# Optimization experiments

Measured on AMD Instinct MI355X. Metric: run time of the kernel, lower is better.

## Reference

```python
import jax, jax.numpy as jnp
import numpy as np

B, NPG, DEG = 128, 400, 16
N, E = B * NPG, B * NPG * DEG
E_PER = E // B
K1, K2, K3 = 360, 324, 292  # ceil(0.9*400), ceil(0.9*360), ceil(0.9*324)
EPS = 1e-5


def setup_inputs() -> dict:
    key = jax.random.key(0)
    ks = jax.random.split(key, 48)
    # edges constrained within each graph (contiguous equal-size graphs)
    g = jnp.repeat(jnp.arange(B, dtype=jnp.int32), E_PER)
    src = jax.random.randint(ks[0], (E,), 0, NPG, dtype=jnp.int32) + g * NPG
    dst = jax.random.randint(ks[1], (E,), 0, NPG, dtype=jnp.int32) + g * NPG
    inp = {
        'x': jax.random.normal(ks[2], (N, 64), dtype=jnp.float32),
        'edge_index': jnp.stack([src, dst]),
        'batch': jnp.repeat(jnp.arange(B, dtype=jnp.int32), NPG),
    }
    def glorot(k, a, b):
        lim = float(np.sqrt(6.0 / (a + b)))
        return jax.random.uniform(k, (a, b), minval=-lim, maxval=lim, dtype=jnp.float32)
    conv_dims = [(64, 32), (32, 64), (64, 128), (128, 128)]
    for i, (a, b) in enumerate(conv_dims, 1):
        inp[f'W{i}'] = glorot(ks[2 + i], a, b)
        inp[f'b{i}'] = jnp.zeros((b,), jnp.float32)
    for i, d in zip((1, 2, 3), (32, 64, 128)):
        inp[f'p{i}'] = jax.random.uniform(ks[8 + i], (d,), minval=-1.0, maxval=1.0, dtype=jnp.float32) / float(np.sqrt(d))
    lin_dims = [(128, 64), (64, 64), (64, 32), (32, 16), (16, 1)]
    for i, (a, b) in enumerate(lin_dims, 1):
        inp[f'Lw{i}'] = glorot(ks[12 + i], a, b)
        inp[f'Lb{i}'] = jnp.zeros((b,), jnp.float32)
    for i, d in enumerate((64, 64, 32, 16), 1):
        inp[f'g{i}'] = jnp.ones((d,), jnp.float32)
        inp[f'be{i}'] = jnp.zeros((d,), jnp.float32)
    return inp


def _gcn(x, src, dst, emask, nmask, W, b):
    h = x @ W
    deg = nmask + jax.ops.segment_sum(emask, dst, num_segments=N)
    dinv = jnp.where(deg > 0, jax.lax.rsqrt(deg), 0.0)
    norm = dinv[src] * dinv[dst] * emask
    agg = jax.ops.segment_sum(h[src] * norm[:, None], dst, num_segments=N)
    agg = agg + h * (dinv * dinv * nmask)[:, None]  # self-loop term
    return (agg + b) * nmask[:, None]


def _topk_pool(x, nmask, p, k):
    # PyG TopKPooling: score = x.p/||p||, keep top-k per graph, x *= tanh(score)
    score = (x @ p) / jnp.linalg.norm(p)
    sel = jnp.where(nmask > 0, score, -jnp.inf).reshape(B, NPG)
    _, idx = jax.lax.top_k(sel, k)
    gidx = (idx + (jnp.arange(B) * NPG)[:, None]).reshape(-1)
    new_mask = jnp.zeros((N,), x.dtype).at[gidx].set(1.0)
    return x * (jnp.tanh(score) * new_mask)[:, None], new_mask


def reference(x, edge_index, batch, W1, b1, p1, W2, b2, p2, W3, b3, p3, W4, b4,
              Lw1, Lb1, Lw2, Lb2, Lw3, Lb3, Lw4, Lb4, Lw5, Lb5,
              g1, be1, g2, be2, g3, be3, g4, be4):
    src, dst = edge_index[0], edge_index[1]
    nmask = jnp.ones((N,), jnp.float32)
    emask = jnp.ones((E,), jnp.float32)
    x = jax.nn.relu(_gcn(x, src, dst, emask, nmask, W1, b1))
    x, nmask = _topk_pool(x, nmask, p1, K1)
    emask = emask * nmask[src] * nmask[dst]
    x = jax.nn.relu(_gcn(x, src, dst, emask, nmask, W2, b2))
    x, nmask = _topk_pool(x, nmask, p2, K2)
    emask = emask * nmask[src] * nmask[dst]
    x = jax.nn.relu(_gcn(x, src, dst, emask, nmask, W3, b3))
    x, nmask = _topk_pool(x, nmask, p3, K3)
    emask = emask * nmask[src] * nmask[dst]
    x = jax.nn.relu(_gcn(x, src, dst, emask, nmask, W4, b4))
    h = x.reshape(B, NPG, -1).max(axis=1)
    def lin_bn(h, W, bb, ga, be):
        h = h @ W + bb
        m = h.mean(0)
        v = h.var(0)  # biased, matches BatchNorm1d training normalization
        return jax.nn.relu(ga * (h - m) / jnp.sqrt(v + EPS) + be)
    h = lin_bn(h, Lw1, Lb1, g1, be1)
    h = lin_bn(h, Lw2, Lb2, g2, be2)
    h = lin_bn(h, Lw3, Lb3, g3, be3)
    h = lin_bn(h, Lw4, Lb4, g4, be4)
    return h @ Lw5 + Lb5
```

## Files before the change

kernel.cpp:

```cpp
#include <hip/hip_runtime.h>
#include <math.h>

#define NNODES 51200
#define BGRAPHS 128
#define NPG 400
#define NEDGES 819200
#define EPG 6400
#define SLP 7680

__global__ __launch_bounds__(512) void csr_build_kernel(
    const int* __restrict__ src, const int* __restrict__ dst,
    unsigned short* __restrict__ slg, int* __restrict__ gsg, int* __restrict__ gcg,
    float* __restrict__ nmask, float* __restrict__ dinv, float* __restrict__ sc,
    float* __restrict__ hp) {
    __shared__ int deg[NPG];
    __shared__ int incl[512];
    __shared__ int gs[NPG];
    __shared__ int cur[NPG];
    const int g = blockIdx.x, t = threadIdx.x;
    for (int i = t; i < NPG; i += 512) deg[i] = 0;
    if (t < 128) hp[g * 128 + t] = 0.0f;
    __syncthreads();
    for (int e = t; e < EPG; e += 512)
        atomicAdd(&deg[dst[g * EPG + e] - g * NPG], 1);
    __syncthreads();
    const int d = (t < NPG) ? deg[t] : 0;
    const int p = (d + 3) >> 2;
    incl[t] = p;
    __syncthreads();
    for (int off = 1; off < 512; off <<= 1) {
        int add = (t >= off) ? incl[t - off] : 0;
        __syncthreads();
        incl[t] += add;
        __syncthreads();
    }
    if (t < NPG) {
        const int gstart = incl[t] - p;
        gs[t] = gstart;
        gsg[g * NPG + t] = gstart;
        gcg[g * NPG + t] = p;
        cur[t] = gstart * 4;
        nmask[g * NPG + t] = 1.0f;
        const float dv = rsqrtf(1.0f + (float)d);
        dinv[g * NPG + t] = dv;
        sc[g * NPG + t] = dv;
    }
    __syncthreads();
    for (int e = t; e < EPG; e += 512) {
        int dl = dst[g * EPG + e] - g * NPG;
        int pos = atomicAdd(&cur[dl], 1);
        slg[g * SLP + pos] = (unsigned short)(src[g * EPG + e] - g * NPG);
    }
    __syncthreads();
    if (t < NPG) {
        const int end = (gs[t] + p) * 4;
        for (int i = cur[t]; i < end; i++) slg[g * SLP + i] = (unsigned short)NPG;
    }
}

template<int IN, int OUT, int MODE>
__global__ __launch_bounds__(256) void gemm_kernel(
    const float* __restrict__ X, const float* __restrict__ W,
    const float* __restrict__ bias, const float* __restrict__ nmask,
    float* __restrict__ H, const float* __restrict__ p,
    float* __restrict__ score, float* __restrict__ hp) {
    __shared__ __align__(16) float sX[64 * IN];
    __shared__ unsigned smax[256];
    const int row0 = blockIdx.x * 64;
    const int t = threadIdx.x;
    for (int i = t; i < 64 * IN / 4; i += 256)
        reinterpret_cast<float4*>(sX)[i] =
            reinterpret_cast<const float4*>(X + (size_t)row0 * IN)[i];
    if (MODE == 3) smax[t] = 0u;
    __syncthreads();
    constexpr int CG  = OUT / 4;
    constexpr int RG  = 256 / CG;
    constexpr int RPT = 64 / RG;
    const int c0 = (t % CG) * 4;
    const int r0 = (t / CG) * RPT;
    float acc[RPT][4];
#pragma unroll
    for (int r = 0; r < RPT; r++)
#pragma unroll
        for (int j = 0; j < 4; j++) acc[r][j] = 0.0f;
    for (int k4 = 0; k4 < IN / 4; k4++) {
        const float4 w0 = *reinterpret_cast<const float4*>(&W[(k4 * 4 + 0) * OUT + c0]);
        const float4 w1 = *reinterpret_cast<const float4*>(&W[(k4 * 4 + 1) * OUT + c0]);
        const float4 w2 = *reinterpret_cast<const float4*>(&W[(k4 * 4 + 2) * OUT + c0]);
        const float4 w3 = *reinterpret_cast<const float4*>(&W[(k4 * 4 + 3) * OUT + c0]);
#pragma unroll
        for (int r = 0; r < RPT; r++) {
            const float4 xv = *reinterpret_cast<const float4*>(&sX[(r0 + r) * IN + k4 * 4]);
            acc[r][0] += xv.x * w0.x + xv.y * w1.x + xv.z * w2.x + xv.w * w3.x;
            acc[r][1] += xv.x * w0.y + xv.y * w1.y + xv.z * w2.y + xv.w * w3.y;
            acc[r][2] += xv.x * w0.z + xv.y * w1.z + xv.z * w2.z + xv.w * w3.z;
            acc[r][3] += xv.x * w0.w + xv.y * w1.w + xv.z * w2.w + xv.w * w3.w;
        }
    }
    const int graph0 = row0 / 400;
    const int bnd = (graph0 + 1) * 400;
    float ps[RPT];
    float cmax[4] = {0.f, 0.f, 0.f, 0.f};
#pragma unroll
    for (int r = 0; r < RPT; r++) {
        const int row = row0 + r0 + r;
        float4 v = make_float4(acc[r][0], acc[r][1], acc[r][2], acc[r][3]);
        if (MODE >= 2) {
            const float4 b4 = *reinterpret_cast<const float4*>(&bias[c0]);
            const float m = nmask[row];
            v.x = fmaxf(v.x + b4.x, 0.0f) * m;
            v.y = fmaxf(v.y + b4.y, 0.0f) * m;
            v.z = fmaxf(v.z + b4.z, 0.0f) * m;
            v.w = fmaxf(v.w + b4.w, 0.0f) * m;
        }
        if (MODE != 3) *reinterpret_cast<float4*>(&H[(size_t)row * OUT + c0]) = v;
        if (MODE == 2) {
            const float4 p4 = *reinterpret_cast<const float4*>(&p[c0]);
            ps[r] = v.x * p4.x + v.y * p4.y + v.z * p4.z + v.w * p4.w;
        }
        if (MODE == 3) {
            cmax[0] = fmaxf(cmax[0], v.x);
            cmax[1] = fmaxf(cmax[1], v.y);
            cmax[2] = fmaxf(cmax[2], v.z);
            cmax[3] = fmaxf(cmax[3], v.w);
        }
    }
    if (MODE == 2) {
#pragma unroll
        for (int r = 0; r < RPT; r++) {
#pragma unroll
            for (int off = 1; off < CG; off <<= 1) ps[r] += __shfl_xor(ps[r], off);
        }
        if ((t % CG) == 0) {
#pragma unroll
            for (int r = 0; r < RPT; r++) score[row0 + r0 + r] = ps[r];
        }
    }
    if (MODE == 3) {
        const int seg = ((row0 + r0) >= bnd) ? 1 : 0;
        atomicMax(&smax[seg * 128 + c0 + 0], __float_as_uint(cmax[0]));
        atomicMax(&smax[seg * 128 + c0 + 1], __float_as_uint(cmax[1]));
        atomicMax(&smax[seg * 128 + c0 + 2], __float_as_uint(cmax[2]));
        atomicMax(&smax[seg * 128 + c0 + 3], __float_as_uint(cmax[3]));
        __syncthreads();
        unsigned* hpu = reinterpret_cast<unsigned*>(hp);
        if (t < 128) atomicMax(&hpu[graph0 * 128 + t], smax[t]);
        const int graph1 = (row0 + 63) / 400;
        if (graph1 != graph0 && t < 128) atomicMax(&hpu[graph1 * 128 + t], smax[128 + t]);
    }
}

template<int OUT, int NCH, int NS, bool EPI, bool SCORE, bool TOPK>
__global__ __launch_bounds__(512) void gcn_agg_kernel(
    const float* __restrict__ H, float* __restrict__ Y,
    const float* __restrict__ dinv_g, const float* __restrict__ sc_g,
    const float* __restrict__ bias,
    const float* __restrict__ p_sc, float* __restrict__ score_out,
    const float* __restrict__ scoreb_in, const float* __restrict__ nmask_in,
    float* __restrict__ nmask_out, const float* __restrict__ p_pool,
    int K, int PDIM,
    const unsigned short* __restrict__ slg, const int* __restrict__ gsg,
    const int* __restrict__ gcg) {
    __shared__ __align__(16) float Hl[(NPG + 1) * 36];
    __shared__ float dinvl[NPG];
    __shared__ float scl[NPG];
    __shared__ int gsl[NPG];
    __shared__ int gcl[NPG];
    __shared__ unsigned long long sl64[SLP / 4];
    __shared__ float misc[4];
    const unsigned short* sl = reinterpret_cast<const unsigned short*>(sl64);
    const int b   = blockIdx.x;
    const int g   = b / (NCH * NS);
    const int rem = b % (NCH * NS);
    const int f0  = (rem / NS) * 32;
    const int n0  = (rem % NS) * (NPG / NS);
    const int t   = threadIdx.x;

    for (int i = t; i < NPG; i += 512) {
        gsl[i] = gsg[g * NPG + i];
        gcl[i] = gcg[g * NPG + i];
    }
    for (int i = t; i < SLP / 4; i += 512)
        sl64[i] = reinterpret_cast<const unsigned long long*>(slg + (size_t)g * SLP)[i];

    if (TOPK) {
        float* sval = Hl;
        int*   sidx = (int*)(Hl + 512);
        float* sraw = Hl + 1024;
        float* nml  = Hl + 1440;
        if (t < 64) {
            float s = 0.0f;
            for (int j = t; j < PDIM; j += 64) s += p_pool[j] * p_pool[j];
#pragma unroll
            for (int o = 32; o > 0; o >>= 1) s += __shfl_xor(s, o, 64);
            if (t == 0) misc[0] = sqrtf(s);
        }
        float v = -INFINITY;
        int ix = t;
        if (t < NPG) {
            const float raw = scoreb_in[g * NPG + t];
            sraw[t] = raw;
            v = (nmask_in[g * NPG + t] > 0.0f) ? raw : -INFINITY;
        }
        __syncthreads();
        for (int kk = 2; kk <= 512; kk <<= 1) {
            for (int j = kk >> 1; j > 0; j >>= 1) {
                float vb; int ib;
                if (j >= 64) {
                    sval[t] = v; sidx[t] = ix;
                    __syncthreads();
                    vb = sval[t ^ j]; ib = sidx[t ^ j];
                    __syncthreads();
                } else {
                    vb = __shfl_xor(v, j, 64);
                    ib = __shfl_xor(ix, j, 64);
                }
                const bool ownFirst = (v > vb) || (v == vb && ix < ib);
                const bool lower = (t & j) == 0;
                const bool desc = (t & kk) == 0;
                const bool keepOwn = lower ? (desc == ownFirst) : (desc != ownFirst);
                if (!keepOwn) { v = vb; ix = ib; }
            }
        }
        if (t <= NPG) nml[t] = 0.0f;
        __syncthreads();
        if (t < K) nml[ix] = 1.0f;
        __syncthreads();
        if (rem == 0 && t < NPG) nmask_out[g * NPG + t] = nml[t];
        const float spn = misc[0];
        for (int n = t; n < NPG; n += 512) {
            float dv = 0.0f;
            if (nml[n] > 0.0f) {
                float d = 1.0f;
                const int g0 = gsl[n], g1 = g0 + gcl[n];
                for (int gg = g0; gg < g1; ++gg) {
                    const unsigned long long q = *reinterpret_cast<const unsigned long long*>(&sl[gg * 4]);
                    d += nml[(int)(q & 0xFFFF)] + nml[(int)((q >> 16) & 0xFFFF)] +
                         nml[(int)((q >> 32) & 0xFFFF)] + nml[(int)(q >> 48)];
                }
                dv = rsqrtf(d);
            }
            dinvl[n] = dv;
            scl[n] = (nml[n] > 0.0f) ? tanhf(sraw[n] / spn) * dv : 0.0f;
        }
        __syncthreads();
    } else {
        for (int i = t; i < NPG; i += 512) {
            dinvl[i] = dinv_g[g * NPG + i];
            scl[i]   = sc_g[g * NPG + i];
        }
        __syncthreads();
    }

    for (int i = t; i < NPG * 8; i += 512) {
        const int n = i >> 3, q = i & 7;
        const float s = scl[n];
        float4 v = *reinterpret_cast<const float4*>(&H[(size_t)(g * NPG + n) * OUT + f0 + q * 4]);
        v.x *= s; v.y *= s; v.z *= s; v.w *= s;
        *reinterpret_cast<float4*>(&Hl[n * 36 + q * 4]) = v;
    }
    if (t < 36) Hl[NPG * 36 + t] = 0.0f;
    __syncthreads();

    const int wave = t >> 6, lane = t & 63;
    const int sub = lane >> 3, f4 = lane & 7;
    constexpr int NPB = NPG / NS;
    for (int n = n0 + wave * 8 + sub; n < n0 + NPB; n += 64) {
        const float di = dinvl[n];
        if (di == 0.0f) continue;
        const int g0 = gsl[n], g1 = g0 + gcl[n];
        float4 acc = *reinterpret_cast<const float4*>(&Hl[n * 36 + f4 * 4]);
        for (int gg = g0; gg < g1; ++gg) {
            const unsigned long long q = *reinterpret_cast<const unsigned long long*>(&sl[gg * 4]);
            const int s0 = (int)(q & 0xFFFF), s1 = (int)((q >> 16) & 0xFFFF);
            const int s2 = (int)((q >> 32) & 0xFFFF), s3 = (int)(q >> 48);
            const float4 a = *reinterpret_cast<const float4*>(&Hl[s0 * 36 + f4 * 4]);
            const float4 bb = *reinterpret_cast<const float4*>(&Hl[s1 * 36 + f4 * 4]);
            const float4 c = *reinterpret_cast<const float4*>(&Hl[s2 * 36 + f4 * 4]);
            const float4 dd = *reinterpret_cast<const float4*>(&Hl[s3 * 36 + f4 * 4]);
            acc.x += (a.x + bb.x) + (c.x + dd.x);
            acc.y += (a.y + bb.y) + (c.y + dd.y);
            acc.z += (a.z + bb.z) + (c.z + dd.z);
            acc.w += (a.w + bb.w) + (c.w + dd.w);
        }
        acc.x *= di; acc.y *= di; acc.z *= di; acc.w *= di;
        if (EPI) {
            const float4 b4 = *reinterpret_cast<const float4*>(&bias[f0 + f4 * 4]);
            acc.x = fmaxf(acc.x + b4.x, 0.0f);
            acc.y = fmaxf(acc.y + b4.y, 0.0f);
            acc.z = fmaxf(acc.z + b4.z, 0.0f);
            acc.w = fmaxf(acc.w + b4.w, 0.0f);
        }
        *reinterpret_cast<float4*>(&Y[(size_t)(g * NPG + n) * OUT + f0 + f4 * 4]) = acc;
        if (SCORE) {
            const float4 p4 = *reinterpret_cast<const float4*>(&p_sc[f4 * 4]);
            float part = acc.x * p4.x + acc.y * p4.y + acc.z * p4.z + acc.w * p4.w;
            part += __shfl_xor(part, 1);
            part += __shfl_xor(part, 2);
            part += __shfl_xor(part, 4);
            if (f4 == 0) score_out[g * NPG + n] = part;
        }
    }
}

template<int IN, int OUT>
__global__ __launch_bounds__(128) void head_layer_kernel(
    const float* __restrict__ A, const float* __restrict__ W,
    const float* __restrict__ b, const float* __restrict__ ga,
    const float* __restrict__ be, float* __restrict__ Y) {
    __shared__ float Al[128 * (IN + 1)];
    __shared__ float red[4];
    const int c = blockIdx.x, t = threadIdx.x;
    for (int i = t; i < 128 * IN; i += 128)
        Al[(i / IN) * (IN + 1) + (i % IN)] = A[i];
    __syncthreads();
    float acc = b[c];
#pragma unroll
    for (int j = 0; j < IN; j++) acc += Al[t * (IN + 1) + j] * W[j * OUT + c];
    float s1 = acc, s2 = acc * acc;
    for (int o = 32; o > 0; o >>= 1) {
        s1 += __shfl_down(s1, o, 64);
        s2 += __shfl_down(s2, o, 64);
    }
    if ((t & 63) == 0) { red[t >> 6] = s1; red[2 + (t >> 6)] = s2; }
    __syncthreads();
    const float S1 = red[0] + red[1], S2 = red[2] + red[3];
    const float m = S1 * (1.0f / 128.0f);
    const float var = S2 * (1.0f / 128.0f) - m * m;
    float val = ga[c] * (acc - m) * rsqrtf(var + 1e-5f) + be[c];
    Y[t * OUT + c] = fmaxf(val, 0.0f);
}

__global__ __launch_bounds__(128) void head_final_kernel(
    const float* __restrict__ A, const float* __restrict__ w,
    const float* __restrict__ b, float* __restrict__ out) {
    const int t = threadIdx.x;
    float acc = b[0];
#pragma unroll
    for (int j = 0; j < 16; j++) acc += A[t * 16 + j] * w[j];
    out[t] = acc;
}

extern "C" void kernel_launch(void* const* d_in, const int* in_sizes, int n_in,
                              void* d_out, int out_size, void* d_ws, size_t ws_size,
                              hipStream_t stream) {
    (void)in_sizes; (void)n_in; (void)out_size; (void)ws_size;
    const float* x   = (const float*)d_in[0];
    const int*   ei  = (const int*)d_in[1];
    const float* W1  = (const float*)d_in[3];  const float* b1  = (const float*)d_in[4];
    const float* W2  = (const float*)d_in[5];  const float* b2  = (const float*)d_in[6];
    const float* W3  = (const float*)d_in[7];  const float* b3  = (const float*)d_in[8];
    const float* W4  = (const float*)d_in[9];  const float* b4  = (const float*)d_in[10];
    const float* p1  = (const float*)d_in[11];
    const float* p2  = (const float*)d_in[12];
    const float* p3  = (const float*)d_in[13];
    const float* Lw1 = (const float*)d_in[14]; const float* Lb1 = (const float*)d_in[15];
    const float* Lw2 = (const float*)d_in[16]; const float* Lb2 = (const float*)d_in[17];
    const float* Lw3 = (const float*)d_in[18]; const float* Lb3 = (const float*)d_in[19];
    const float* Lw4 = (const float*)d_in[20]; const float* Lb4 = (const float*)d_in[21];
    const float* Lw5 = (const float*)d_in[22]; const float* Lb5 = (const float*)d_in[23];
    const float* g1  = (const float*)d_in[24]; const float* be1 = (const float*)d_in[25];
    const float* g2  = (const float*)d_in[26]; const float* be2 = (const float*)d_in[27];
    const float* g3  = (const float*)d_in[28]; const float* be3 = (const float*)d_in[29];
    const float* g4  = (const float*)d_in[30]; const float* be4 = (const float*)d_in[31];

    const int* src = ei;
    const int* dst = ei + NEDGES;

    float* ws    = (float*)d_ws;
    float* hb    = ws;
    float* x0    = hb + (size_t)NNODES * 128;
    float* x1    = x0 + (size_t)NNODES * 128;
    float* nmA   = x1 + (size_t)NNODES * 128;
    float* nmB   = nmA + NNODES;
    float* dinv  = nmB + NNODES;
    float* sc    = dinv + NNODES;
    float* scoreb= sc + NNODES;
    float* hp    = scoreb + NNODES;
    float* a1    = hp + 128 * 128;
    float* a2    = a1 + 128 * 64;
    float* a3    = a2 + 128 * 64;
    float* a4    = a3 + 128 * 32;
    unsigned short* slg = (unsigned short*)(a4 + 128 * 16);
    int* gsg = (int*)(slg + (size_t)BGRAPHS * SLP);
    int* gcg = gsg + (size_t)BGRAPHS * NPG;

    csr_build_kernel<<<BGRAPHS, 512, 0, stream>>>(src, dst, slg, gsg, gcg, nmA, dinv, sc, hp);

    gemm_kernel<64, 32, 0><<<NNODES / 64, 256, 0, stream>>>(x, W1, nullptr, nullptr, hb, nullptr, nullptr, nullptr);
    gcn_agg_kernel<32, 1, 2, true, true, false><<<BGRAPHS * 2, 512, 0, stream>>>(
        hb, x0, dinv, sc, b1, p1, scoreb,
        nullptr, nullptr, nullptr, nullptr, 0, 0, slg, gsg, gcg);

    gcn_agg_kernel<32, 1, 2, false, false, true><<<BGRAPHS * 2, 512, 0, stream>>>(
        x0, hb, nullptr, nullptr, nullptr, nullptr, nullptr,
        scoreb, nmA, nmB, p1, 360, 32, slg, gsg, gcg);
    gemm_kernel<32, 64, 2><<<NNODES / 64, 256, 0, stream>>>(hb, W2, b2, nmB, x1, p2, scoreb, nullptr);

    gcn_agg_kernel<64, 2, 2, false, false, true><<<BGRAPHS * 4, 512, 0, stream>>>(
        x1, hb, nullptr, nullptr, nullptr, nullptr, nullptr,
        scoreb, nmB, nmA, p2, 324, 64, slg, gsg, gcg);
    gemm_kernel<64, 128, 2><<<NNODES / 64, 256, 0, stream>>>(hb, W3, b3, nmA, x0, p3, scoreb, nullptr);

    gcn_agg_kernel<128, 4, 1, false, false, true><<<BGRAPHS * 4, 512, 0, stream>>>(
        x0, hb, nullptr, nullptr, nullptr, nullptr, nullptr,
        scoreb, nmA, nmB, p3, 292, 128, slg, gsg, gcg);
    gemm_kernel<128, 128, 3><<<NNODES / 64, 256, 0, stream>>>(hb, W4, b4, nmB, x1, nullptr, nullptr, hp);

    head_layer_kernel<128, 64><<<64, 128, 0, stream>>>(hp, Lw1, Lb1, g1, be1, a1);
    head_layer_kernel<64, 64><<<64, 128, 0, stream>>>(a1, Lw2, Lb2, g2, be2, a2);
    head_layer_kernel<64, 32><<<32, 128, 0, stream>>>(a2, Lw3, Lb3, g3, be3, a3);
    head_layer_kernel<32, 16><<<16, 128, 0, stream>>>(a3, Lw4, Lb4, g4, be4, a4);
    head_final_kernel<<<1, 128, 0, stream>>>(a4, Lw5, Lb5, (float*)d_out);
}
```

Measured before the change: 197.1 us.

## Fuse conv2 pooling/aggregation with W2 GEMM and merge head tail layers

Adds a conv2 fused kernel that does the top-k pool, degree normalisation, neighbour aggregation and the 32x64 GEMM with bias, ReLU and score in one block per half-graph. The aggregated result stays in shared memory, so the intermediate write/read of hb and one launch are removed. The order changes from GEMM-then-aggregate to aggregate-then-GEMM, which is linear and therefore equivalent. Score buffers are double-buffered to avoid aliasing. The last three head layers (two linear+BN and the final linear) are merged into one single-block kernel to cut launch overhead. The cost is that the top-k sort and degree computation are now repeated in both half-graph blocks.

```diff
diff --git a/kernel.cpp b/kernel.cpp
--- a/kernel.cpp
+++ b/kernel.cpp
@@ -7,6 +7,9 @@
 #define NEDGES 819200
 #define EPG 6400
 #define SLP 7680
+
+__device__ __forceinline__ float4 ld4(const float* p) { return *reinterpret_cast<const float4*>(p); }
+__device__ __forceinline__ void st4(float* p, float4 v) { *reinterpret_cast<float4*>(p) = v; }
 
 __global__ __launch_bounds__(512) void csr_build_kernel(
     const int* __restrict__ src, const int* __restrict__ dst,
@@ -84,13 +87,13 @@
 #pragma unroll
         for (int j = 0; j < 4; j++) acc[r][j] = 0.0f;
     for (int k4 = 0; k4 < IN / 4; k4++) {
-        const float4 w0 = *reinterpret_cast<const float4*>(&W[(k4 * 4 + 0) * OUT + c0]);
-        const float4 w1 = *reinterpret_cast<const float4*>(&W[(k4 * 4 + 1) * OUT + c0]);
-        const float4 w2 = *reinterpret_cast<const float4*>(&W[(k4 * 4 + 2) * OUT + c0]);
-        const float4 w3 = *reinterpret_cast<const float4*>(&W[(k4 * 4 + 3) * OUT + c0]);
+        const float4 w0 = ld4(&W[(k4 * 4 + 0) * OUT + c0]);
+        const float4 w1 = ld4(&W[(k4 * 4 + 1) * OUT + c0]);
+        const float4 w2 = ld4(&W[(k4 * 4 + 2) * OUT + c0]);
+        const float4 w3 = ld4(&W[(k4 * 4 + 3) * OUT + c0]);
 #pragma unroll
         for (int r = 0; r < RPT; r++) {
-            const float4 xv = *reinterpret_cast<const float4*>(&sX[(r0 + r) * IN + k4 * 4]);
+            const float4 xv = ld4(&sX[(r0 + r) * IN + k4 * 4]);
             acc[r][0] += xv.x * w0.x + xv.y * w1.x + xv.z * w2.x + xv.w * w3.x;
             acc[r][1] += xv.x * w0.y + xv.y * w1.y + xv.z * w2.y + xv.w * w3.y;
             acc[r][2] += xv.x * w0.z + xv.y * w1.z + xv.z * w2.z + xv.w * w3.z;
@@ -106,16 +109,16 @@
         const int row = row0 + r0 + r;
         float4 v = make_float4(acc[r][0], acc[r][1], acc[r][2], acc[r][3]);
         if (MODE >= 2) {
-            const float4 b4 = *reinterpret_cast<const float4*>(&bias[c0]);
+            const float4 b4 = ld4(&bias[c0]);
             const float m = nmask[row];
             v.x = fmaxf(v.x + b4.x, 0.0f) * m;
             v.y = fmaxf(v.y + b4.y, 0.0f) * m;
             v.z = fmaxf(v.z + b4.z, 0.0f) * m;
             v.w = fmaxf(v.w + b4.w, 0.0f) * m;
         }
-        if (MODE != 3) *reinterpret_cast<float4*>(&H[(size_t)row * OUT + c0]) = v;
+        if (MODE != 3) st4(&H[(size_t)row * OUT + c0], v);
         if (MODE == 2) {
-            const float4 p4 = *reinterpret_cast<const float4*>(&p[c0]);
+            const float4 p4 = ld4(&p[c0]);
             ps[r] = v.x * p4.x + v.y * p4.y + v.z * p4.z + v.w * p4.w;
         }
         if (MODE == 3) {
@@ -255,9 +258,9 @@
     for (int i = t; i < NPG * 8; i += 512) {
         const int n = i >> 3, q = i & 7;
         const float s = scl[n];
-        float4 v = *reinterpret_cast<const float4*>(&H[(size_t)(g * NPG + n) * OUT + f0 + q * 4]);
+        float4 v = ld4(&H[(size_t)(g * NPG + n) * OUT + f0 + q * 4]);
         v.x *= s; v.y *= s; v.z *= s; v.w *= s;
-        *reinterpret_cast<float4*>(&Hl[n * 36 + q * 4]) = v;
+        st4(&Hl[n * 36 + q * 4], v);
     }
     if (t < 36) Hl[NPG * 36 + t] = 0.0f;
     __syncthreads();
@@ -269,15 +272,15 @@
         const float di = dinvl[n];
         if (di == 0.0f) continue;
         const int g0 = gsl[n], g1 = g0 + gcl[n];
-        float4 acc = *reinterpret_cast<const float4*>(&Hl[n * 36 + f4 * 4]);
+        float4 acc = ld4(&Hl[n * 36 + f4 * 4]);
         for (int gg = g0; gg < g1; ++gg) {
             const unsigned long long q = *reinterpret_cast<const unsigned long long*>(&sl[gg * 4]);
             const int s0 = (int)(q & 0xFFFF), s1 = (int)((q >> 16) & 0xFFFF);
             const int s2 = (int)((q >> 32) & 0xFFFF), s3 = (int)(q >> 48);
-            const float4 a = *reinterpret_cast<const float4*>(&Hl[s0 * 36 + f4 * 4]);
-            const float4 bb = *reinterpret_cast<const float4*>(&Hl[s1 * 36 + f4 * 4]);
-            const float4 c = *reinterpret_cast<const float4*>(&Hl[s2 * 36 + f4 * 4]);
-            const float4 dd = *reinterpret_cast<const float4*>(&Hl[s3 * 36 + f4 * 4]);
+            const float4 a = ld4(&Hl[s0 * 36 + f4 * 4]);
+            const float4 bb = ld4(&Hl[s1 * 36 + f4 * 4]);
+            const float4 c = ld4(&Hl[s2 * 36 + f4 * 4]);
+            const float4 dd = ld4(&Hl[s3 * 36 + f4 * 4]);
             acc.x += (a.x + bb.x) + (c.x + dd.x);
             acc.y += (a.y + bb.y) + (c.y + dd.y);
             acc.z += (a.z + bb.z) + (c.z + dd.z);
@@ -285,20 +288,181 @@
         }
         acc.x *= di; acc.y *= di; acc.z *= di; acc.w *= di;
         if (EPI) {
-            const float4 b4 = *reinterpret_cast<const float4*>(&bias[f0 + f4 * 4]);
+            const float4 b4 = ld4(&bias[f0 + f4 * 4]);
             acc.x = fmaxf(acc.x + b4.x, 0.0f);
             acc.y = fmaxf(acc.y + b4.y, 0.0f);
             acc.z = fmaxf(acc.z + b4.z, 0.0f);
             acc.w = fmaxf(acc.w + b4.w, 0.0f);
         }
-        *reinterpret_cast<float4*>(&Y[(size_t)(g * NPG + n) * OUT + f0 + f4 * 4]) = acc;
+        st4(&Y[(size_t)(g * NPG + n) * OUT + f0 + f4 * 4], acc);
         if (SCORE) {
-            const float4 p4 = *reinterpret_cast<const float4*>(&p_sc[f4 * 4]);
+            const float4 p4 = ld4(&p_sc[f4 * 4]);
             float part = acc.x * p4.x + acc.y * p4.y + acc.z * p4.z + acc.w * p4.w;
             part += __shfl_xor(part, 1);
             part += __shfl_xor(part, 2);
             part += __shfl_xor(part, 4);
             if (f4 == 0) score_out[g * NPG + n] = part;
+        }
+    }
+}
+
+__global__ __launch_bounds__(512) void conv2_fused_kernel(
+    const float* __restrict__ X0, float* __restrict__ X1,
+    const float* __restrict__ scoreb_in, const float* __restrict__ nmask_in,
+    float* __restrict__ nmask_out, float* __restrict__ scoreb_out,
+    const float* __restrict__ p_pool,
+    const float* __restrict__ W2, const float* __restrict__ b2,
+    const float* __restrict__ p2,
+    const unsigned short* __restrict__ slg, const int* __restrict__ gsg,
+    const int* __restrict__ gcg) {
+    __shared__ __align__(16) float Hl[(NPG + 1) * 36];
+    __shared__ __align__(16) float out2[200 * 36];
+    __shared__ float dinvl[NPG];
+    __shared__ float scl[NPG];
+    __shared__ int gsl[NPG];
+    __shared__ int gcl[NPG];
+    __shared__ unsigned long long sl64[SLP / 4];
+    __shared__ float misc[4];
+    const unsigned short* sl = reinterpret_cast<const unsigned short*>(sl64);
+    const int b = blockIdx.x, g = b >> 1, seg = b & 1;
+    const int n0 = seg * 200;
+    const int t = threadIdx.x;
+
+    for (int i = t; i < NPG; i += 512) {
+        gsl[i] = gsg[g * NPG + i];
+        gcl[i] = gcg[g * NPG + i];
+    }
+    for (int i = t; i < SLP / 4; i += 512)
+        sl64[i] = reinterpret_cast<const unsigned long long*>(slg + (size_t)g * SLP)[i];
+
+    {
+        float* sval = Hl;
+        int*   sidx = (int*)(Hl + 512);
+        float* sraw = Hl + 1024;
+        float* nml  = Hl + 1440;
+        if (t < 64) {
+            float s = 0.0f;
+            for (int j = t; j < 32; j += 64) s += p_pool[j] * p_pool[j];
+#pragma unroll
+            for (int o = 32; o > 0; o >>= 1) s += __shfl_xor(s, o, 64);
+            if (t == 0) misc[0] = sqrtf(s);
+        }
+        float v = -INFINITY;
+        int ix = t;
+        if (t < NPG) {
+            const float raw = scoreb_in[g * NPG + t];
+            sraw[t] = raw;
+            v = (nmask_in[g * NPG + t] > 0.0f) ? raw : -INFINITY;
+        }
+        __syncthreads();
+        for (int kk = 2; kk <= 512; kk <<= 1) {
+            for (int j = kk >> 1; j > 0; j >>= 1) {
+                float vb; int ib;
+                if (j >= 64) {
+                    sval[t] = v; sidx[t] = ix;
+                    __syncthreads();
+                    vb = sval[t ^ j]; ib = sidx[t ^ j];
+                    __syncthreads();
+                } else {
+                    vb = __shfl_xor(v, j, 64);
+                    ib = __shfl_xor(ix, j, 64);
+                }
+                const bool ownFirst = (v > vb) || (v == vb && ix < ib);
+                const bool lower = (t & j) == 0;
+                const bool desc = (t & kk) == 0;
+                const bool keepOwn = lower ? (desc == ownFirst) : (desc != ownFirst);
+                if (!keepOwn) { v = vb; ix = ib; }
+            }
+        }
+        if (t <= NPG) nml[t] = 0.0f;
+        __syncthreads();
+        if (t < 360) nml[ix] = 1.0f;
+        __syncthreads();
+        if (seg == 0 && t < NPG) nmask_out[g * NPG + t] = nml[t];
+        const float spn = misc[0];
+        for (int n = t; n < NPG; n += 512) {
+            float dv = 0.0f;
+            if (nml[n] > 0.0f) {
+                float d = 1.0f;
+                const int g0 = gsl[n], g1 = g0 + gcl[n];
+                for (int gg = g0; gg < g1; ++gg) {
+                    const unsigned long long q = *reinterpret_cast<const unsigned long long*>(&sl[gg * 4]);
+                    d += nml[(int)(q & 0xFFFF)] + nml[(int)((q >> 16) & 0xFFFF)] +
+                         nml[(int)((q >> 32) & 0xFFFF)] + nml[(int)(q >> 48)];
+                }
+                dv = rsqrtf(d);
+            }
+            dinvl[n] = dv;
+            scl[n] = (nml[n] > 0.0f) ? tanhf(sraw[n] / spn) * dv : 0.0f;
+        }
+        __syncthreads();
+    }
+
+    for (int i = t; i < NPG * 8; i += 512) {
+        const int n = i >> 3, q = i & 7;
+        const float s = scl[n];
+        float4 v = ld4(&X0[(size_t)(g * NPG + n) * 32 + q * 4]);
+        v.x *= s; v.y *= s; v.z *= s; v.w *= s;
+        st4(&Hl[n * 36 + q * 4], v);
+    }
+    if (t < 36) Hl[NPG * 36 + t] = 0.0f;
+    __syncthreads();
+
+    {
+        const int wave = t >> 6, lane = t & 63;
+        const int sub = lane >> 3, f4 = lane & 7;
+        for (int n = n0 + wave * 8 + sub; n < n0 + 200; n += 64) {
+            const float di = dinvl[n];
+            float4 acc = make_float4(0.f, 0.f, 0.f, 0.f);
+            if (di != 0.0f) {
+                acc = ld4(&Hl[n * 36 + f4 * 4]);
+                const int g0 = gsl[n], g1 = g0 + gcl[n];
+                for (int gg = g0; gg < g1; ++gg) {
+                    const unsigned long long q = *reinterpret_cast<const unsigned long long*>(&sl[gg * 4]);
+                    const int s0 = (int)(q & 0xFFFF), s1 = (int)((q >> 16) & 0xFFFF);
+                    const int s2 = (int)((q >> 32) & 0xFFFF), s3 = (int)(q >> 48);
+                    const float4 a = ld4(&Hl[s0 * 36 + f4 * 4]);
+                    const float4 bb = ld4(&Hl[s1 * 36 + f4 * 4]);
+                    const float4 c = ld4(&Hl[s2 * 36 + f4 * 4]);
+                    const float4 dd = ld4(&Hl[s3 * 36 + f4 * 4]);
+                    acc.x += (a.x + bb.x) + (c.x + dd.x);
+                    acc.y += (a.y + bb.y) + (c.y + dd.y);
+                    acc.z += (a.z + bb.z) + (c.z + dd.z);
+                    acc.w += (a.w + bb.w) + (c.w + dd.w);
+                }
+                acc.x *= di; acc.y *= di; acc.z *= di; acc.w *= di;
+            }
+            st4(&out2[(n - n0) * 36 + f4 * 4], acc);
+        }
+    }
+    __syncthreads();
+
+    {
+        const int c0 = (t & 15) * 4;
+        const int slot = t >> 4;
+        for (int n = n0 + slot; n < n0 + 200; n += 32) {
+            float a0 = 0.f, a1 = 0.f, a2 = 0.f, a3 = 0.f;
+            for (int k4 = 0; k4 < 8; k4++) {
+                const float4 w0 = ld4(&W2[(k4 * 4 + 0) * 64 + c0]);
+                const float4 w1 = ld4(&W2[(k4 * 4 + 1) * 64 + c0]);
+                const float4 w2 = ld4(&W2[(k4 * 4 + 2) * 64 + c0]);
+                const float4 w3 = ld4(&W2[(k4 * 4 + 3) * 64 + c0]);
+                const float4 xv = ld4(&out2[(n - n0) * 36 + k4 * 4]);
+                a0 += xv.x * w0.x + xv.y * w1.x + xv.z * w2.x + xv.w * w3.x;
+                a1 += xv.x * w0.y + xv.y * w1.y + xv.z * w2.y + xv.w * w3.y;
+                a2 += xv.x * w0.z + xv.y * w1.z + xv.z * w2.z + xv.w * w3.z;
+                a3 += xv.x * w0.w + xv.y * w1.w + xv.z * w2.w + xv.w * w3.w;
+            }
+            const float m = (dinvl[n] > 0.0f) ? 1.0f : 0.0f;
+            const float4 bb = ld4(&b2[c0]);
+            float4 v = make_float4(fmaxf(a0 + bb.x, 0.f) * m, fmaxf(a1 + bb.y, 0.f) * m,
+                                   fmaxf(a2 + bb.z, 0.f) * m, fmaxf(a3 + bb.w, 0.f) * m);
+            st4(&X1[(size_t)(g * NPG + n) * 64 + c0], v);
+            const float4 p4 = ld4(&p2[c0]);
+            float ps = v.x * p4.x + v.y * p4.y + v.z * p4.z + v.w * p4.w;
+            ps += __shfl_xor(ps, 1); ps += __shfl_xor(ps, 2);
+            ps += __shfl_xor(ps, 4); ps += __shfl_xor(ps, 8);
+            if ((t & 15) == 0) scoreb_out[g * NPG + n] = ps;
         }
     }
 }
@@ -331,14 +495,80 @@
     Y[t * OUT + c] = fmaxf(val, 0.0f);
 }
 
-__global__ __launch_bounds__(128) void head_final_kernel(
-    const float* __restrict__ A, const float* __restrict__ w,
-    const float* __restrict__ b, float* __restrict__ out) {
+__global__ __launch_bounds__(512) void head_tail_kernel(
+    const float* __restrict__ A2,
+    const float* __restrict__ Lw3, const float* __restrict__ Lb3,
+    const float* __restrict__ g3, const float* __restrict__ be3,
+    const float* __restrict__ Lw4, const float* __restrict__ Lb4,
+    const float* __restrict__ g4, const float* __restrict__ be4,
+    const float* __restrict__ Lw5, const float* __restrict__ Lb5,
+    float* __restrict__ out) {
+    __shared__ __align__(16) float A[128 * 68];
+    __shared__ __align__(16) float Z[128 * 36];
+    __shared__ __align__(16) float Z2[128 * 20];
+    __shared__ float mv[64];
     const int t = threadIdx.x;
-    float acc = b[0];
-#pragma unroll
-    for (int j = 0; j < 16; j++) acc += A[t * 16 + j] * w[j];
-    out[t] = acc;
+    for (int i = t; i < 128 * 16; i += 512) {
+        const int r = i >> 4, q = i & 15;
+        st4(&A[r * 68 + q * 4], ld4(&A2[r * 64 + q * 4]));
+    }
+    __syncthreads();
+    {
+        const int c = t & 31, rs = t >> 5;
+        for (int r = rs; r < 128; r += 16) {
+            float acc = Lb3[c];
+            for (int j4 = 0; j4 < 16; j4++) {
+                const float4 a = ld4(&A[r * 68 + j4 * 4]);
+                acc += a.x * Lw3[(j4 * 4 + 0) * 32 + c] + a.y * Lw3[(j4 * 4 + 1) * 32 + c]
+                     + a.z * Lw3[(j4 * 4 + 2) * 32 + c] + a.w * Lw3[(j4 * 4 + 3) * 32 + c];
+            }
+            Z[r * 36 + c] = acc;
+        }
+    }
+    __syncthreads();
+    if (t < 32) {
+        float s1 = 0.f, s2 = 0.f;
+        for (int r = 0; r < 128; r++) { const float v = Z[r * 36 + t]; s1 += v; s2 += v * v; }
+        const float m = s1 * (1.0f / 128.0f);
+        mv[t] = m; mv[32 + t] = s2 * (1.0f / 128.0f) - m * m;
+    }
+    __syncthreads();
+    {
+        const int c = t & 31;
+        const float m = mv[c], scn = g3[c] * rsqrtf(mv[32 + c] + 1e-5f), bb = be3[c];
+        for (int r = t >> 5; r < 128; r += 16)
+            Z[r * 36 + c] = fmaxf((Z[r * 36 + c] - m) * scn + bb, 0.f);
+    }
+    __syncthreads();
+    {
+        const int c = t & 15, rs = t >> 4;
+        for (int r = rs; r < 128; r += 32) {
+            float acc = Lb4[c];
+            for (int j4 = 0; j4 < 8; j4++) {
+                const float4 a = ld4(&Z[r * 36 + j4 * 4]);
+                acc += a.x * Lw4[(j4 * 4 + 0) * 16 + c] + a.y * Lw4[(j4 * 4 + 1) * 16 + c]
+                     + a.z * Lw4[(j4 * 4 + 2) * 16 + c] + a.w * Lw4[(j4 * 4 + 3) * 16 + c];
+            }
+            Z2[r * 20 + c] = acc;
+        }
+    }
+    __syncthreads();
+    if (t < 16) {
+        float s1 = 0.f, s2 = 0.f;
+        for (int r = 0; r < 128; r++) { const float v = Z2[r * 20 + t]; s1 += v; s2 += v * v; }
+        const float m = s1 * (1.0f / 128.0f);
+        mv[t] = m; mv[32 + t] = s2 * (1.0f / 128.0f) - m * m;
+    }
+    __syncthreads();
+    if (t < 128) {
+        float acc = Lb5[0];
+#pragma unroll
+        for (int j = 0; j < 16; j++) {
+            const float v = fmaxf((Z2[t * 20 + j] - mv[j]) * (g4[j] * rsqrtf(mv[32 + j] + 1e-5f)) + be4[j], 0.f);
+            acc += v * Lw5[j];
+        }
+        out[t] = acc;
+    }
 }
 
 extern "C" void kernel_launch(void* const* d_in, const int* in_sizes, int n_in,
@@ -375,13 +605,12 @@
     float* nmB   = nmA + NNODES;
     float* dinv  = nmB + NNODES;
     float* sc    = dinv + NNODES;
-    float* scoreb= sc + NNODES;
-    float* hp    = scoreb + NNODES;
+    float* scbA  = sc + NNODES;
+    float* scbB  = scbA + NNODES;
+    float* hp    = scbB + NNODES;
     float* a1    = hp + 128 * 128;
     float* a2    = a1 + 128 * 64;
-    float* a3    = a2 + 128 * 64;
-    float* a4    = a3 + 128 * 32;
-    unsigned short* slg = (unsigned short*)(a4 + 128 * 16);
+    unsigned short* slg = (unsigned short*)(a2 + 128 * 64);
     int* gsg = (int*)(slg + (size_t)BGRAPHS * SLP);
     int* gcg = gsg + (size_t)BGRAPHS * NPG;
 
@@ -389,27 +618,23 @@
 
     gemm_kernel<64, 32, 0><<<NNODES / 64, 256, 0, stream>>>(x, W1, nullptr, nullptr, hb, nullptr, nullptr, nullptr);
     gcn_agg_kernel<32, 1, 2, true, true, false><<<BGRAPHS * 2, 512, 0, stream>>>(
-        hb, x0, dinv, sc, b1, p1, scoreb,
+        hb, x0, dinv, sc, b1, p1, scbA,
         nullptr, nullptr, nullptr, nullptr, 0, 0, slg, gsg, gcg);
 
-    gcn_agg_kernel<32, 1, 2, false, false, true><<<BGRAPHS * 2, 512, 0, stream>>>(
-        x0, hb, nullptr, nullptr, nullptr, nullptr, nullptr,
-        scoreb, nmA, nmB, p1, 360, 32, slg, gsg, gcg);
-    gemm_kernel<32, 64, 2><<<NNODES / 64, 256, 0, stream>>>(hb, W2, b2, nmB, x1, p2, scoreb, nullptr);
+    conv2_fused_kernel<<<BGRAPHS * 2, 512, 0, stream>>>(
+        x0, x1, scbA, nmA, nmB, scbB, p1, W2, b2, p2, slg, gsg, gcg);
 
     gcn_agg_kernel<64, 2, 2, false, false, true><<<BGRAPHS * 4, 512, 0, stream>>>(
         x1, hb, nullptr, nullptr, nullptr, nullptr, nullptr,
-        scoreb, nmB, nmA, p2, 324, 64, slg, gsg, gcg);
-    gemm_kernel<64, 128, 2><<<NNODES / 64, 256, 0, stream>>>(hb, W3, b3, nmA, x0, p3, scoreb, nullptr);
+        scbB, nmB, nmA, p2, 324, 64, slg, gsg, gcg);
+    gemm_kernel<64, 128, 2><<<NNODES / 64, 256, 0, stream>>>(hb, W3, b3, nmA, x0, p3, scbA, nullptr);
 
     gcn_agg_kernel<128, 4, 1, false, false, true><<<BGRAPHS * 4, 512, 0, stream>>>(
         x0, hb, nullptr, nullptr, nullptr, nullptr, nullptr,
-        scoreb, nmA, nmB, p3, 292, 128, slg, gsg, gcg);
+        scbA, nmA, nmB, p3, 292, 128, slg, gsg, gcg);
     gemm_kernel<128, 128, 3><<<NNODES / 64, 256, 0, stream>>>(hb, W4, b4, nmB, x1, nullptr, nullptr, hp);
 
     head_layer_kernel<128, 64><<<64, 128, 0, stream>>>(hp, Lw1, Lb1, g1, be1, a1);
     head_layer_kernel<64, 64><<<64, 128, 0, stream>>>(a1, Lw2, Lb2, g2, be2, a2);
-    head_layer_kernel<64, 32><<<32, 128, 0, stream>>>(a2, Lw3, Lb3, g3, be3, a3);
-    head_layer_kernel<32, 16><<<16, 128, 0, stream>>>(a3, Lw4, Lb4, g4, be4, a4);
-    head_final_kernel<<<1, 128, 0, stream>>>(a4, Lw5, Lb5, (float*)d_out);
+    head_tail_kernel<<<1, 512, 0, stream>>>(a2, Lw3, Lb3, g3, be3, Lw4, Lb4, g4, be4, Lw5, Lb5, (float*)d_out);
 }
```

Result: faster. 192.4 us, median of 3 (-2.4%).
